# Kernel optimization log

Hardware: AMD Instinct MI355X
Metric: run time of the kernel (lower is better)

Reference implementation:

```python
import jax, jax.numpy as jnp
import numpy as np


def setup_inputs() -> dict:
    key = jax.random.key(0)
    k1, k2 = jax.random.split(key)
    K, C, D = 72, 1024, 128   # num_codebooks, codebook_size, codebook_dim
    B, T = 16, 2048
    embs = jax.random.normal(k1, (K, C, D), dtype=jnp.float32)
    r = jax.random.normal(k2, (B, T, D), dtype=jnp.float32)
    code = jnp.zeros((B, T, K), dtype=jnp.int64)
    return {"embs": embs, "r": r, "code": code}


def reference(embs, r, code):
    """Residual multi-codebook VQ encode (depthsum_encoding_step).

    embs: [K, C, D] codebooks; r: [B, T, D] residual; code: [B, T, K] int64.
    Per depth i: dist = ||e||^2 - 2 r.e  (argmin equivalent to full sq dist),
    idx = argmin_c dist, r <- r - embs[i][idx], code[..., i] = idx.
    Sequential dependence across depths -> lax.scan over the K axis.
    """
    def step(r, e):  # e: [C, D]
        # [B, T, C] distance surrogate (||r||^2 omitted: constant in argmin)
        dist = jnp.sum(e * e, axis=-1) - 2.0 * jnp.einsum("btd,cd->btc", r, e)
        idx = jnp.argmin(dist, axis=-1)           # [B, T]
        r = r - e[idx]                            # gather + residual update
        return r, idx

    _, idxs = jax.lax.scan(step, r, embs)         # idxs: [K, B, T]
    code = jnp.moveaxis(idxs, 0, -1).astype(code.dtype)  # [B, T, K]
    return code
```

## Files before the change

### kernel.cpp

```cpp
#include <hip/hip_runtime.h>
#include <float.h>

#define KDEP 72
#define CSZ  1024
#define DDIM 128
#define MT   64
#define TILE_CW 64
#define NTILES 16
#define NTHREADS 256
#define NBLK 512

typedef float f32x2 __attribute__((ext_vector_type(2)));
typedef float f32x4 __attribute__((ext_vector_type(4)));

#define PK_FMA_LO(acc, rp, ep) \
    asm("v_pk_fma_f32 %0, %1, %2, %0 op_sel:[0,0,0] op_sel_hi:[1,0,1]" \
        : "+v"(acc) : "v"(rp), "v"(ep))
#define PK_FMA_HI(acc, rp, ep) \
    asm("v_pk_fma_f32 %0, %1, %2, %0 op_sel:[0,1,0] op_sel_hi:[1,1,1]" \
        : "+v"(acc) : "v"(rp), "v"(ep))

__global__ void ee_precompute(const float* __restrict__ embs,
                              float* __restrict__ ee_out)
{
    const int k = blockIdx.x;
    const float* ek = embs + (size_t)k * (CSZ * DDIM);
    #pragma unroll
    for (int q = 0; q < 4; ++q) {
        const int cw = q * NTHREADS + threadIdx.x;
        const float4* ev = (const float4*)(ek + (size_t)cw * DDIM);
        float r8[8];
        #pragma unroll
        for (int j = 0; j < 8; ++j) r8[j] = 0.0f;
        for (int i = 0; i < 16; ++i) {
            float4 va = ev[2 * i];
            float4 vb = ev[2 * i + 1];
            float p0 = va.x * va.x; asm volatile("" : "+v"(p0));
            float p1 = va.y * va.y; asm volatile("" : "+v"(p1));
            float p2 = va.z * va.z; asm volatile("" : "+v"(p2));
            float p3 = va.w * va.w; asm volatile("" : "+v"(p3));
            float p4 = vb.x * vb.x; asm volatile("" : "+v"(p4));
            float p5 = vb.y * vb.y; asm volatile("" : "+v"(p5));
            float p6 = vb.z * vb.z; asm volatile("" : "+v"(p6));
            float p7 = vb.w * vb.w; asm volatile("" : "+v"(p7));
            r8[0] += p0; r8[1] += p1; r8[2] += p2; r8[3] += p3;
            r8[4] += p4; r8[5] += p5; r8[6] += p6; r8[7] += p7;
        }
        ee_out[(size_t)k * CSZ + cw] = ((r8[0] + r8[1]) + (r8[2] + r8[3]))
                                     + ((r8[4] + r8[5]) + (r8[6] + r8[7]));
    }
}

__launch_bounds__(NTHREADS, 2)
__global__ void rvq_encode_f32(const float* __restrict__ embs,
                               const float* __restrict__ r_in,
                               const float* __restrict__ ee_ws,
                               int* __restrict__ code_out)
{
    __shared__ __align__(16) float rt[DDIM][MT];
    __shared__ float4 e32[TILE_CW * 33];
    __shared__ float  eeL[CSZ];
    __shared__ float  mrg_m[MT][16];
    __shared__ int    mrg_i[MT][16];
    __shared__ int    idxd[MT];

    const int tid  = threadIdx.x;
    const int tg   = tid >> 4;
    const int cg   = tid & 15;
    const int tok0 = tg * 4;
    const long gtok0 = (long)blockIdx.x * MT;

    {
        const int tok = tid >> 2, q = tid & 3;
        const float4* rsrc = (const float4*)(r_in + (size_t)(gtok0 + tok) * DDIM) + q * 8;
        #pragma unroll
        for (int t = 0; t < 8; ++t) {
            float4 f = rsrc[t];
            const int d = q * 32 + t * 4;
            rt[d + 0][tok] = f.x; rt[d + 1][tok] = f.y;
            rt[d + 2][tok] = f.z; rt[d + 3][tok] = f.w;
        }
    }

    for (int k = 0; k < KDEP; ++k) {
        const float* ek = embs + (size_t)k * (CSZ * DDIM);

        ((float4*)eeL)[tid] = ((const float4*)(ee_ws + (size_t)k * CSZ))[tid];

        float m1[4];
        int   i1[4];
        #pragma unroll
        for (int i = 0; i < 4; ++i) { m1[i] = FLT_MAX; i1[i] = 0; }

        for (int tile = 0; tile < NTILES; ++tile) {
            const int c0 = tile * TILE_CW;
            __syncthreads();

            {
                const float4* gsrc = (const float4*)(ek + (size_t)c0 * DDIM);
                #pragma unroll
                for (int it = 0; it < 8; ++it) {
                    int u  = it * NTHREADS + tid;
                    int cw = u >> 5, c4 = u & 31;
                    e32[cw * 33 + c4] = gsrc[u];
                }
            }
            __syncthreads();

            f32x2 acc[2][4];
            #pragma unroll
            for (int ip = 0; ip < 2; ++ip)
                #pragma unroll
                for (int j = 0; j < 4; ++j) acc[ip][j] = (f32x2)(0.0f);

            #pragma unroll 2
            for (int dg = 0; dg < 32; ++dg) {
                f32x4 rv[4];
                f32x4 ev[4];
                #pragma unroll
                for (int dd = 0; dd < 4; ++dd)
                    rv[dd] = *(const f32x4*)&rt[dg * 4 + dd][tok0];
                #pragma unroll
                for (int j = 0; j < 4; ++j)
                    ev[j] = *(const f32x4*)&e32[(cg + j * 16) * 33 + dg];

                #pragma unroll
                for (int dd = 0; dd < 4; ++dd) {
                    f32x2 rp0 = __builtin_shufflevector(rv[dd], rv[dd], 0, 1);
                    f32x2 rp1 = __builtin_shufflevector(rv[dd], rv[dd], 2, 3);
                    #pragma unroll
                    for (int j = 0; j < 4; ++j) {
                        f32x2 ep = (dd < 2)
                            ? __builtin_shufflevector(ev[j], ev[j], 0, 1)
                            : __builtin_shufflevector(ev[j], ev[j], 2, 3);
                        if (dd & 1) {
                            PK_FMA_HI(acc[0][j], rp0, ep);
                            PK_FMA_HI(acc[1][j], rp1, ep);
                        } else {
                            PK_FMA_LO(acc[0][j], rp0, ep);
                            PK_FMA_LO(acc[1][j], rp1, ep);
                        }
                    }
                }
            }

            #pragma unroll
            for (int j = 0; j < 4; ++j) {
                const int   c  = c0 + cg + j * 16;
                const float ee = eeL[c];
                float d0 = __builtin_fmaf(-2.0f, acc[0][j].x, ee);
                float d1 = __builtin_fmaf(-2.0f, acc[0][j].y, ee);
                float d2 = __builtin_fmaf(-2.0f, acc[1][j].x, ee);
                float d3 = __builtin_fmaf(-2.0f, acc[1][j].y, ee);
                if (d0 < m1[0]) { m1[0] = d0; i1[0] = c; }
                if (d1 < m1[1]) { m1[1] = d1; i1[1] = c; }
                if (d2 < m1[2]) { m1[2] = d2; i1[2] = c; }
                if (d3 < m1[3]) { m1[3] = d3; i1[3] = c; }
            }
        }

        #pragma unroll
        for (int i = 0; i < 4; ++i) {
            mrg_m[tok0 + i][cg] = m1[i];
            mrg_i[tok0 + i][cg] = i1[i];
        }
        __syncthreads();
        if (tid < MT) {
            float gm = FLT_MAX;
            int   gi = 0x7fffffff;
            for (int g = 0; g < 16; ++g) {
                float em = mrg_m[tid][g];
                int   ei = mrg_i[tid][g];
                if (em < gm || (em == gm && ei < gi)) { gm = em; gi = ei; }
            }
            idxd[tid] = gi;
            code_out[(size_t)(gtok0 + tid) * KDEP + k] = gi;
        }
        __syncthreads();

        {
            const int tok = tid >> 2, q = tid & 3;
            const int idx = idxd[tok];
            const float4* ev = (const float4*)(ek + (size_t)idx * DDIM) + q * 8;
            #pragma unroll
            for (int t = 0; t < 8; ++t) {
                float4 f = ev[t];
                const int d = q * 32 + t * 4;
                rt[d + 0][tok] -= f.x;
                rt[d + 1][tok] -= f.y;
                rt[d + 2][tok] -= f.z;
                rt[d + 3][tok] -= f.w;
            }
        }
    }
}

extern "C" void kernel_launch(void* const* d_in, const int* in_sizes, int n_in,
                              void* d_out, int out_size, void* d_ws, size_t ws_size,
                              hipStream_t stream) {
    (void)in_sizes; (void)n_in; (void)ws_size; (void)out_size;
    const float* embs = (const float*)d_in[0];
    const float* r    = (const float*)d_in[1];
    float* ee = (float*)d_ws;
    int* out = (int*)d_out;
    hipLaunchKernelGGL(ee_precompute, dim3(KDEP), dim3(NTHREADS), 0, stream,
                       embs, ee);
    hipLaunchKernelGGL(rvq_encode_f32, dim3(NBLK), dim3(NTHREADS), 0, stream,
                       embs, r, ee, out);
}
```

Baseline: 8.370 ms.

## Enlarge register tile to 8x8 with 128-token blocks and 128-codeword tiles

Doubles tokens per block and codewords per shared-memory tile so each thread computes an 8x8 tile of dot products instead of 4x4. This raises FMA-per-LDS-load intensity and halves tile loads per codebook. In exchange the block uses much more LDS and registers, runs one block per CU with half as many blocks, and loses inter-block latency hiding around barriers.

Measured after the change: 7.648 ms. 8.6% less time.

```diff
diff --git a/kernel.cpp b/kernel.cpp
--- a/kernel.cpp
+++ b/kernel.cpp
@@ -4,11 +4,11 @@
 #define KDEP 72
 #define CSZ  1024
 #define DDIM 128
-#define MT   64
-#define TILE_CW 64
-#define NTILES 16
+#define MT   128
+#define TILE_CW 128
+#define NTILES 8
 #define NTHREADS 256
-#define NBLK 512
+#define NBLK 256
 
 typedef float f32x2 __attribute__((ext_vector_type(2)));
 typedef float f32x4 __attribute__((ext_vector_type(4)));
@@ -51,14 +51,14 @@
     }
 }
 
-__launch_bounds__(NTHREADS, 2)
+__launch_bounds__(NTHREADS, 1)
 __global__ void rvq_encode_f32(const float* __restrict__ embs,
                                const float* __restrict__ r_in,
                                const float* __restrict__ ee_ws,
                                int* __restrict__ code_out)
 {
     __shared__ __align__(16) float rt[DDIM][MT];
-    __shared__ float4 e32[TILE_CW * 33];
+    __shared__ float4 et[TILE_CW * 33];
     __shared__ float  eeL[CSZ];
     __shared__ float  mrg_m[MT][16];
     __shared__ int    mrg_i[MT][16];
@@ -67,16 +67,16 @@
     const int tid  = threadIdx.x;
     const int tg   = tid >> 4;
     const int cg   = tid & 15;
-    const int tok0 = tg * 4;
+    const int tok0 = tg * 8;
     const long gtok0 = (long)blockIdx.x * MT;
 
     {
-        const int tok = tid >> 2, q = tid & 3;
-        const float4* rsrc = (const float4*)(r_in + (size_t)(gtok0 + tok) * DDIM) + q * 8;
-        #pragma unroll
-        for (int t = 0; t < 8; ++t) {
+        const int tok = tid >> 1, half = tid & 1;
+        const float4* rsrc = (const float4*)(r_in + (size_t)(gtok0 + tok) * DDIM) + half * 16;
+        #pragma unroll
+        for (int t = 0; t < 16; ++t) {
             float4 f = rsrc[t];
-            const int d = q * 32 + t * 4;
+            const int d = half * 64 + t * 4;
             rt[d + 0][tok] = f.x; rt[d + 1][tok] = f.y;
             rt[d + 2][tok] = f.z; rt[d + 3][tok] = f.w;
         }
@@ -87,10 +87,10 @@
 
         ((float4*)eeL)[tid] = ((const float4*)(ee_ws + (size_t)k * CSZ))[tid];
 
-        float m1[4];
-        int   i1[4];
-        #pragma unroll
-        for (int i = 0; i < 4; ++i) { m1[i] = FLT_MAX; i1[i] = 0; }
+        float m1[8];
+        int   i1[8];
+        #pragma unroll
+        for (int i = 0; i < 8; ++i) { m1[i] = FLT_MAX; i1[i] = 0; }
 
         for (int tile = 0; tile < NTILES; ++tile) {
             const int c0 = tile * TILE_CW;
@@ -99,68 +99,72 @@
             {
                 const float4* gsrc = (const float4*)(ek + (size_t)c0 * DDIM);
                 #pragma unroll
-                for (int it = 0; it < 8; ++it) {
+                for (int it = 0; it < 16; ++it) {
                     int u  = it * NTHREADS + tid;
                     int cw = u >> 5, c4 = u & 31;
-                    e32[cw * 33 + c4] = gsrc[u];
+                    et[cw * 33 + c4] = gsrc[u];
                 }
             }
             __syncthreads();
 
-            f32x2 acc[2][4];
+            f32x2 acc[4][8];
             #pragma unroll
-            for (int ip = 0; ip < 2; ++ip)
-                #pragma unroll
-                for (int j = 0; j < 4; ++j) acc[ip][j] = (f32x2)(0.0f);
+            for (int p = 0; p < 4; ++p)
+                #pragma unroll
+                for (int j = 0; j < 8; ++j) acc[p][j] = (f32x2)(0.0f);
 
             #pragma unroll 2
             for (int dg = 0; dg < 32; ++dg) {
-                f32x4 rv[4];
-                f32x4 ev[4];
-                #pragma unroll
-                for (int dd = 0; dd < 4; ++dd)
-                    rv[dd] = *(const f32x4*)&rt[dg * 4 + dd][tok0];
-                #pragma unroll
-                for (int j = 0; j < 4; ++j)
-                    ev[j] = *(const f32x4*)&e32[(cg + j * 16) * 33 + dg];
+                f32x4 ev[8];
+                #pragma unroll
+                for (int j = 0; j < 8; ++j)
+                    ev[j] = *(const f32x4*)&et[(cg + j * 16) * 33 + dg];
 
                 #pragma unroll
                 for (int dd = 0; dd < 4; ++dd) {
-                    f32x2 rp0 = __builtin_shufflevector(rv[dd], rv[dd], 0, 1);
-                    f32x2 rp1 = __builtin_shufflevector(rv[dd], rv[dd], 2, 3);
+                    const int d = dg * 4 + dd;
+                    f32x4 rva = *(const f32x4*)&rt[d][tok0];
+                    f32x4 rvb = *(const f32x4*)&rt[d][tok0 + 4];
+                    f32x2 rp0 = __builtin_shufflevector(rva, rva, 0, 1);
+                    f32x2 rp1 = __builtin_shufflevector(rva, rva, 2, 3);
+                    f32x2 rp2 = __builtin_shufflevector(rvb, rvb, 0, 1);
+                    f32x2 rp3 = __builtin_shufflevector(rvb, rvb, 2, 3);
                     #pragma unroll
-                    for (int j = 0; j < 4; ++j) {
+                    for (int j = 0; j < 8; ++j) {
                         f32x2 ep = (dd < 2)
                             ? __builtin_shufflevector(ev[j], ev[j], 0, 1)
                             : __builtin_shufflevector(ev[j], ev[j], 2, 3);
                         if (dd & 1) {
                             PK_FMA_HI(acc[0][j], rp0, ep);
                             PK_FMA_HI(acc[1][j], rp1, ep);
+                            PK_FMA_HI(acc[2][j], rp2, ep);
+                            PK_FMA_HI(acc[3][j], rp3, ep);
                         } else {
                             PK_FMA_LO(acc[0][j], rp0, ep);
                             PK_FMA_LO(acc[1][j], rp1, ep);
+                            PK_FMA_LO(acc[2][j], rp2, ep);
+                            PK_FMA_LO(acc[3][j], rp3, ep);
                         }
                     }
                 }
             }
 
             #pragma unroll
-            for (int j = 0; j < 4; ++j) {
+            for (int j = 0; j < 8; ++j) {
                 const int   c  = c0 + cg + j * 16;
                 const float ee = eeL[c];
-                float d0 = __builtin_fmaf(-2.0f, acc[0][j].x, ee);
-                float d1 = __builtin_fmaf(-2.0f, acc[0][j].y, ee);
-                float d2 = __builtin_fmaf(-2.0f, acc[1][j].x, ee);
-                float d3 = __builtin_fmaf(-2.0f, acc[1][j].y, ee);
-                if (d0 < m1[0]) { m1[0] = d0; i1[0] = c; }
-                if (d1 < m1[1]) { m1[1] = d1; i1[1] = c; }
-                if (d2 < m1[2]) { m1[2] = d2; i1[2] = c; }
-                if (d3 < m1[3]) { m1[3] = d3; i1[3] = c; }
-            }
-        }
-
-        #pragma unroll
-        for (int i = 0; i < 4; ++i) {
+                #pragma unroll
+                for (int p = 0; p < 4; ++p) {
+                    float dlo = __builtin_fmaf(-2.0f, acc[p][j].x, ee);
+                    float dhi = __builtin_fmaf(-2.0f, acc[p][j].y, ee);
+                    if (dlo < m1[2 * p])     { m1[2 * p] = dlo;     i1[2 * p] = c; }
+                    if (dhi < m1[2 * p + 1]) { m1[2 * p + 1] = dhi; i1[2 * p + 1] = c; }
+                }
+            }
+        }
+
+        #pragma unroll
+        for (int i = 0; i < 8; ++i) {
             mrg_m[tok0 + i][cg] = m1[i];
             mrg_i[tok0 + i][cg] = i1[i];
         }
@@ -179,13 +183,13 @@
         __syncthreads();
 
         {
-            const int tok = tid >> 2, q = tid & 3;
+            const int tok = tid >> 1, half = tid & 1;
             const int idx = idxd[tok];
-            const float4* ev = (const float4*)(ek + (size_t)idx * DDIM) + q * 8;
+            const float4* ev4 = (const float4*)(ek + (size_t)idx * DDIM) + half * 16;
             #pragma unroll
-            for (int t = 0; t < 8; ++t) {
-                float4 f = ev[t];
-                const int d = q * 32 + t * 4;
+            for (int t = 0; t < 16; ++t) {
+                float4 f = ev4[t];
+                const int d = half * 64 + t * 4;
                 rt[d + 0][tok] -= f.x;
                 rt[d + 1][tok] -= f.y;
                 rt[d + 2][tok] -= f.z;
```
